# Performance work log

Hardware: AMD Instinct MI355X
Metric: run time of the kernel (lower is better)

The kernel has to match this reference:

```python
import jax, jax.numpy as jnp
import numpy as np

N = 50000      # nodes
E = 1_000_000  # edges (avg degree 20)
D = 64         # hidden dim
L = 3          # num dynamics layers
LN_EPS = 1e-5


def layernorm(h, g, b):
    mu = jnp.mean(h, axis=-1, keepdims=True)
    var = jnp.mean(jnp.square(h - mu), axis=-1, keepdims=True)
    return (h - mu) * jax.lax.rsqrt(var + LN_EPS) * g + b


def transformer_conv(h, src, dst, Wq, bq, Wk, bk, Wv, bv, Ws, bs):
    # PyG TransformerConv, heads=1, concat=False, beta=False, root_weight=True
    n = h.shape[0]
    d = Wq.shape[1]
    q = h @ Wq + bq            # [N, D] queries (dst side)
    k = h @ Wk + bk            # [N, D] keys   (src side)
    v = h @ Wv + bv            # [N, D] values (src side)
    logits = jnp.sum(q[dst] * k[src], axis=-1) / jnp.sqrt(jnp.asarray(d, h.dtype))  # [E]
    # segment softmax over incoming edges of each dst node
    m = jax.ops.segment_max(logits, dst, num_segments=n)      # [N]
    e = jnp.exp(logits - m[dst])                               # [E]
    s = jax.ops.segment_sum(e, dst, num_segments=n)            # [N]
    a = e / s[dst]                                             # [E]
    agg = jax.ops.segment_sum(a[:, None] * v[src], dst, num_segments=n)  # [N, D]
    return agg + h @ Ws + bs   # root/skip connection


def setup_inputs() -> dict:
    key = jax.random.key(0)
    ks = jax.random.split(key, 24)
    w = lambda k, shape: (jax.random.normal(k, shape, jnp.float32) * 0.05)
    inp = {
        "x": jax.random.normal(ks[0], (N, D), jnp.float32),
        "edge_index": jax.random.randint(ks[1], (2, E), 0, N, jnp.int32),
        # input_proj conv params
        "Wq0": w(ks[2], (D, D)), "bq0": w(ks[3], (D,)),
        "Wk0": w(ks[4], (D, D)), "bk0": w(ks[5], (D,)),
        "Wv0": w(ks[6], (D, D)), "bv0": w(ks[7], (D,)),
        "Ws0": w(ks[8], (D, D)), "bs0": w(ks[9], (D,)),
        "ln0_g": jnp.ones((D,), jnp.float32), "ln0_b": jnp.zeros((D,), jnp.float32),
        # stacked dynamics conv params [L, ...]
        "Wq": w(ks[10], (L, D, D)), "bq": w(ks[11], (L, D)),
        "Wk": w(ks[12], (L, D, D)), "bk": w(ks[13], (L, D)),
        "Wv": w(ks[14], (L, D, D)), "bv": w(ks[15], (L, D)),
        "Ws": w(ks[16], (L, D, D)), "bs": w(ks[17], (L, D)),
        "ln_g": jnp.ones((L, D), jnp.float32), "ln_b": jnp.zeros((L, D), jnp.float32),
    }
    return inp


def reference(x, edge_index, Wq0, bq0, Wk0, bk0, Wv0, bv0, Ws0, bs0, ln0_g, ln0_b,
              Wq, bq, Wk, bk, Wv, bv, Ws, bs, ln_g, ln_b):
    src, dst = edge_index[0], edge_index[1]
    h = transformer_conv(x, src, dst, Wq0, bq0, Wk0, bk0, Wv0, bv0, Ws0, bs0)
    h = jax.nn.relu(layernorm(h, ln0_g, ln0_b))
    # dropout is identity in eval mode
    for i in range(L):
        hi = transformer_conv(h, src, dst, Wq[i], bq[i], Wk[i], bk[i],
                              Wv[i], bv[i], Ws[i], bs[i])
        h = jax.nn.relu(layernorm(hi + h, ln_g[i], ln_b[i]))
    return h
```

## Files before the change

### kernel.cpp

```cpp
#include <hip/hip_runtime.h>
#include <math.h>

#define NN 50000
#define NE 1000000
#define CAP 64
#define LN_EPS 1e-5f
#define ROW_TILES 3125
#define BE_T 250112

typedef __attribute__((ext_vector_type(8))) short short8;
typedef __attribute__((ext_vector_type(8))) unsigned short ushort8;
typedef __attribute__((ext_vector_type(4))) float f32x4;

__device__ __forceinline__ unsigned short f2bf(float f) {
  union { float f; unsigned u; } v; v.f = f;
  unsigned r = v.u + 0x7FFF + ((v.u >> 16) & 1);
  return (unsigned short)(r >> 16);
}
__device__ __forceinline__ float bf2f(unsigned short b) {
  union { unsigned u; float f; } v; v.u = ((unsigned)b) << 16;
  return v.f;
}

__global__ __launch_bounds__(256) void build_ell(const int* __restrict__ ei,
                                                 int* __restrict__ cursor,
                                                 unsigned short* __restrict__ ell) {
  int t = blockIdx.x * 256 + threadIdx.x;
  int e[4]; bool v[4]; int s[4], d[4], p[4];
#pragma unroll
  for (int i = 0; i < 4; ++i) { e[i] = t + i * BE_T; v[i] = e[i] < NE; }
#pragma unroll
  for (int i = 0; i < 4; ++i) {
    if (v[i]) { s[i] = ei[e[i]]; d[i] = ei[NE + e[i]]; }
  }
#pragma unroll
  for (int i = 0; i < 4; ++i) {
    if (v[i]) p[i] = atomicAdd(&cursor[d[i]], 1);
  }
#pragma unroll
  for (int i = 0; i < 4; ++i) {
    if (v[i] && p[i] < CAP) ell[(size_t)d[i] * CAP + p[i]] = (unsigned short)s[i];
  }
}

__global__ __launch_bounds__(256) void wprep(
    const float* __restrict__ Wq0, const float* __restrict__ bq0,
    const float* __restrict__ Wk0, const float* __restrict__ bk0,
    const float* __restrict__ Wv0, const float* __restrict__ bv0,
    const float* __restrict__ Ws0, const float* __restrict__ bs0,
    const float* __restrict__ WqL, const float* __restrict__ bqL,
    const float* __restrict__ WkL, const float* __restrict__ bkL,
    const float* __restrict__ WvL, const float* __restrict__ bvL,
    const float* __restrict__ WsL, const float* __restrict__ bsL,
    unsigned short* __restrict__ Wt, float* __restrict__ Bc) {
  int tid = blockIdx.x * 256 + threadIdx.x;
  if (tid >= 4 * 256 * 64) return;
  int lyr = tid >> 14;
  int rem = tid & 16383;
  int c = rem >> 6;
  int k = rem & 63;
  int m = c >> 6;
  int n = c & 63;
  const float *W, *B;
  if (lyr == 0) {
    const float* Wm[4] = {Wq0, Wk0, Wv0, Ws0};
    const float* Bm[4] = {bq0, bk0, bv0, bs0};
    W = Wm[m]; B = Bm[m];
  } else {
    const float* Wm[4] = {WqL, WkL, WvL, WsL};
    const float* Bm[4] = {bqL, bkL, bvL, bsL};
    W = Wm[m] + (size_t)(lyr - 1) * 4096;
    B = Bm[m] + (size_t)(lyr - 1) * 64;
  }
  Wt[(size_t)lyr * 16384 + (size_t)c * 64 + k] = f2bf(W[(size_t)k * 64 + n]);
  if (k == 0) Bc[lyr * 256 + c] = B[n];
}

__global__ __launch_bounds__(256) void gemm_qkvs(
    const float* __restrict__ h, const unsigned short* __restrict__ Wt,
    const float* __restrict__ Bc, float* __restrict__ Qf,
    unsigned int* __restrict__ KVb, float* __restrict__ Sf) {
  __shared__ unsigned short lw[256 * 72];
  int tid = threadIdx.x;
#pragma unroll
  for (int it = 0; it < 8; ++it) {
    int id = it * 256 + tid;
    int row = id >> 3, cc = id & 7;
    float4 src = *reinterpret_cast<const float4*>(Wt + (size_t)row * 64 + cc * 8);
    *reinterpret_cast<float4*>(lw + (size_t)row * 72 + cc * 8) = src;
  }
  __syncthreads();

  int wave = tid >> 6, lane = tid & 63;
  int tile = blockIdx.x * 4 + wave;
  if (tile >= ROW_TILES) return;
  int lo = lane & 15, hi = lane >> 4;
  int row = tile * 16 + lo;
  const float* hrow = h + (size_t)row * 64;

  auto packA = [&](const float* p) {
    float4 x = *reinterpret_cast<const float4*>(p);
    float4 y = *reinterpret_cast<const float4*>(p + 4);
    short8 r;
    r[0] = (short)f2bf(x.x); r[1] = (short)f2bf(x.y);
    r[2] = (short)f2bf(x.z); r[3] = (short)f2bf(x.w);
    r[4] = (short)f2bf(y.x); r[5] = (short)f2bf(y.y);
    r[6] = (short)f2bf(y.z); r[7] = (short)f2bf(y.w);
    return r;
  };
  short8 a0 = packA(hrow + hi * 8);
  short8 a1 = packA(hrow + 32 + hi * 8);

  int rb = tile * 16 + hi * 4;

  auto mm = [&](int brow, float bias) {
    f32x4 acc = {bias, bias, bias, bias};
    const unsigned short* wr = lw + (size_t)brow * 72 + hi * 8;
    short8 b0 = *reinterpret_cast<const short8*>(wr);
    short8 b1 = *reinterpret_cast<const short8*>(wr + 32);
    acc = __builtin_amdgcn_mfma_f32_16x16x32_bf16(a0, b0, acc, 0, 0, 0);
    acc = __builtin_amdgcn_mfma_f32_16x16x32_bf16(a1, b1, acc, 0, 0, 0);
    return acc;
  };

#pragma unroll
  for (int ct = 0; ct < 4; ++ct) {
    int col = ct * 16 + lo;
    f32x4 acc = mm(col, Bc[col]);
#pragma unroll
    for (int r = 0; r < 4; ++r) Qf[(size_t)(rb + r) * 64 + col] = acc[r];
  }
#pragma unroll
  for (int cg = 0; cg < 4; ++cg) {
    int col = cg * 16 + lo;
    f32x4 aK = mm(64 + col, Bc[64 + col]);
    f32x4 aV = mm(128 + col, Bc[128 + col]);
#pragma unroll
    for (int r = 0; r < 4; ++r) {
      unsigned int pk = (unsigned int)f2bf(aK[r]) | ((unsigned int)f2bf(aV[r]) << 16);
      KVb[(size_t)(rb + r) * 64 + col] = pk;
    }
  }
#pragma unroll
  for (int ct = 0; ct < 4; ++ct) {
    int col = ct * 16 + lo;
    f32x4 acc = mm(192 + col, Bc[192 + col]);
#pragma unroll
    for (int r = 0; r < 4; ++r) Sf[(size_t)(rb + r) * 64 + col] = acc[r];
  }
}

__global__ __launch_bounds__(256) void edge_fused(
    const float* __restrict__ Qf, const unsigned short* __restrict__ KVb,
    const float* __restrict__ Sf,
    const unsigned short* __restrict__ ell, const int* __restrict__ cursor,
    const float* __restrict__ ln_g, const float* __restrict__ ln_b,
    const float* __restrict__ h_res, float* __restrict__ h_out, int use_res) {
  int node = blockIdx.x * 4 + (threadIdx.x >> 6);
  if (node >= NN) return;
  int lane = threadIdx.x & 63;
  int g = lane >> 4, t = lane & 15;

  int deg = cursor[node];
  if (deg > CAP) deg = CAP;
  const unsigned short* lst = ell + (size_t)node * CAP;

  float4 q4 = *reinterpret_cast<const float4*>(Qf + (size_t)node * 64 + t * 4);

  float4 acc = {0.f, 0.f, 0.f, 0.f};
  float ssum = 0.f;
  int passes = (deg + 3) >> 2;
  for (int p = 0; p < passes; ++p) {
    int slot = p * 4 + g;
    bool valid = slot < deg;
    int src = valid ? (int)lst[slot] : 0;
    ushort8 kv = *reinterpret_cast<const ushort8*>(KVb + (size_t)src * 128 + t * 8);
    float dp = q4.x * bf2f(kv[0]) + q4.y * bf2f(kv[2]) +
               q4.z * bf2f(kv[4]) + q4.w * bf2f(kv[6]);
    dp += __shfl_xor(dp, 1, 64);
    dp += __shfl_xor(dp, 2, 64);
    dp += __shfl_xor(dp, 4, 64);
    dp += __shfl_xor(dp, 8, 64);
    float w = valid ? __expf(dp * 0.125f) : 0.f;
    ssum += w;
    acc.x = fmaf(w, bf2f(kv[1]), acc.x);
    acc.y = fmaf(w, bf2f(kv[3]), acc.y);
    acc.z = fmaf(w, bf2f(kv[5]), acc.z);
    acc.w = fmaf(w, bf2f(kv[7]), acc.w);
  }
#pragma unroll
  for (int off = 16; off <= 32; off <<= 1) {
    acc.x += __shfl_xor(acc.x, off, 64);
    acc.y += __shfl_xor(acc.y, off, 64);
    acc.z += __shfl_xor(acc.z, off, 64);
    acc.w += __shfl_xor(acc.w, off, 64);
    ssum  += __shfl_xor(ssum, off, 64);
  }
  float inv = (ssum > 0.f) ? (1.f / ssum) : 0.f;

  float4 s4 = *reinterpret_cast<const float4*>(Sf + (size_t)node * 64 + t * 4);
  float4 o;
  o.x = acc.x * inv + s4.x;
  o.y = acc.y * inv + s4.y;
  o.z = acc.z * inv + s4.z;
  o.w = acc.w * inv + s4.w;
  if (use_res) {
    float4 r4 = *reinterpret_cast<const float4*>(h_res + (size_t)node * 64 + t * 4);
    o.x += r4.x; o.y += r4.y; o.z += r4.z; o.w += r4.w;
  }

  float sum = o.x + o.y + o.z + o.w;
  sum += __shfl_xor(sum, 1, 64);
  sum += __shfl_xor(sum, 2, 64);
  sum += __shfl_xor(sum, 4, 64);
  sum += __shfl_xor(sum, 8, 64);
  float mu = sum * (1.f / 64.f);
  float dx = o.x - mu, dy = o.y - mu, dz = o.z - mu, dw = o.w - mu;
  float vs = dx * dx + dy * dy + dz * dz + dw * dw;
  vs += __shfl_xor(vs, 1, 64);
  vs += __shfl_xor(vs, 2, 64);
  vs += __shfl_xor(vs, 4, 64);
  vs += __shfl_xor(vs, 8, 64);
  float rstd = rsqrtf(vs * (1.f / 64.f) + LN_EPS);
  float4 gg = *reinterpret_cast<const float4*>(ln_g + t * 4);
  float4 bb = *reinterpret_cast<const float4*>(ln_b + t * 4);
  float4 y;
  y.x = fmaxf(dx * rstd * gg.x + bb.x, 0.f);
  y.y = fmaxf(dy * rstd * gg.y + bb.y, 0.f);
  y.z = fmaxf(dz * rstd * gg.z + bb.z, 0.f);
  y.w = fmaxf(dw * rstd * gg.w + bb.w, 0.f);
  *reinterpret_cast<float4*>(h_out + (size_t)node * 64 + t * 4) = y;
}

extern "C" void kernel_launch(void* const* d_in, const int* in_sizes, int n_in,
                              void* d_out, int out_size, void* d_ws, size_t ws_size,
                              hipStream_t stream) {
  const float* x    = (const float*)d_in[0];
  const int*   ei   = (const int*)d_in[1];
  const float* Wq0  = (const float*)d_in[2];
  const float* bq0  = (const float*)d_in[3];
  const float* Wk0  = (const float*)d_in[4];
  const float* bk0  = (const float*)d_in[5];
  const float* Wv0  = (const float*)d_in[6];
  const float* bv0  = (const float*)d_in[7];
  const float* Ws0  = (const float*)d_in[8];
  const float* bs0  = (const float*)d_in[9];
  const float* ln0g = (const float*)d_in[10];
  const float* ln0b = (const float*)d_in[11];
  const float* WqL  = (const float*)d_in[12];
  const float* bqL  = (const float*)d_in[13];
  const float* WkL  = (const float*)d_in[14];
  const float* bkL  = (const float*)d_in[15];
  const float* WvL  = (const float*)d_in[16];
  const float* bvL  = (const float*)d_in[17];
  const float* WsL  = (const float*)d_in[18];
  const float* bsL  = (const float*)d_in[19];
  const float* lnG  = (const float*)d_in[20];
  const float* lnB  = (const float*)d_in[21];

  float* h = (float*)d_out;

  char* ws = (char*)d_ws;
  size_t off = 0;
  float* Qf = (float*)(ws + off);                    off += (size_t)NN * 64 * 4;
  float* Sf = (float*)(ws + off);                    off += (size_t)NN * 64 * 4;
  unsigned int* KVb = (unsigned int*)(ws + off);     off += (size_t)NN * 128 * 2;
  unsigned short* ell = (unsigned short*)(ws + off); off += (size_t)NN * CAP * 2;
  int* cursor = (int*)(ws + off);                    off += (size_t)NN * 4;
  unsigned short* Wt = (unsigned short*)(ws + off);  off += (size_t)4 * 256 * 64 * 2;
  float* Bc = (float*)(ws + off);                    off += (size_t)4 * 256 * 4;

  hipMemsetAsync(cursor, 0, NN * sizeof(int), stream);
  build_ell<<<BE_T / 256, 256, 0, stream>>>(ei, cursor, ell);
  wprep<<<256, 256, 0, stream>>>(Wq0, bq0, Wk0, bk0, Wv0, bv0, Ws0, bs0,
                                 WqL, bqL, WkL, bkL, WvL, bvL, WsL, bsL, Wt, Bc);

  for (int layer = 0; layer < 4; ++layer) {
    const float* hin = (layer == 0) ? x : h;
    const float* lg = (layer == 0) ? ln0g : lnG + (size_t)(layer - 1) * 64;
    const float* lb = (layer == 0) ? ln0b : lnB + (size_t)(layer - 1) * 64;
    gemm_qkvs<<<(ROW_TILES + 3) / 4, 256, 0, stream>>>(
        hin, Wt + (size_t)layer * 16384, Bc + (size_t)layer * 256, Qf, KVb, Sf);
    edge_fused<<<(NN + 3) / 4, 256, 0, stream>>>(
        Qf, (const unsigned short*)KVb, Sf, ell, cursor, lg, lb, h, h,
        layer > 0 ? 1 : 0);
  }
}
```

Before: 423.7 us.

## Fuse ELL build into first GEMM, store Q as bf16, prefetch KV

Merges the edge-list build into the layer-0 QKVS GEMM launch as extra blocks, so graph construction can overlap with the projection and one launch is dropped. Queries are now stored in bf16 instead of fp32, halving Q traffic. The edge aggregation loop software-pipelines neighbor K/V loads two passes ahead to hide gather latency. The costs are lower precision in the attention logits and higher register pressure in the edge kernel.

```diff
diff --git a/kernel.cpp b/kernel.cpp
--- a/kernel.cpp
+++ b/kernel.cpp
@@ -6,7 +6,9 @@
 #define CAP 64
 #define LN_EPS 1e-5f
 #define ROW_TILES 3125
+#define GEMM_BLOCKS 782
 #define BE_T 250112
+#define ELL_BLOCKS 977
 
 typedef __attribute__((ext_vector_type(8))) short short8;
 typedef __attribute__((ext_vector_type(8))) unsigned short ushort8;
@@ -20,27 +22,6 @@
 __device__ __forceinline__ float bf2f(unsigned short b) {
   union { unsigned u; float f; } v; v.u = ((unsigned)b) << 16;
   return v.f;
-}
-
-__global__ __launch_bounds__(256) void build_ell(const int* __restrict__ ei,
-                                                 int* __restrict__ cursor,
-                                                 unsigned short* __restrict__ ell) {
-  int t = blockIdx.x * 256 + threadIdx.x;
-  int e[4]; bool v[4]; int s[4], d[4], p[4];
-#pragma unroll
-  for (int i = 0; i < 4; ++i) { e[i] = t + i * BE_T; v[i] = e[i] < NE; }
-#pragma unroll
-  for (int i = 0; i < 4; ++i) {
-    if (v[i]) { s[i] = ei[e[i]]; d[i] = ei[NE + e[i]]; }
-  }
-#pragma unroll
-  for (int i = 0; i < 4; ++i) {
-    if (v[i]) p[i] = atomicAdd(&cursor[d[i]], 1);
-  }
-#pragma unroll
-  for (int i = 0; i < 4; ++i) {
-    if (v[i] && p[i] < CAP) ell[(size_t)d[i] * CAP + p[i]] = (unsigned short)s[i];
-  }
 }
 
 __global__ __launch_bounds__(256) void wprep(
@@ -78,10 +59,33 @@
 
 __global__ __launch_bounds__(256) void gemm_qkvs(
     const float* __restrict__ h, const unsigned short* __restrict__ Wt,
-    const float* __restrict__ Bc, float* __restrict__ Qf,
-    unsigned int* __restrict__ KVb, float* __restrict__ Sf) {
+    const float* __restrict__ Bc, unsigned short* __restrict__ Qb,
+    unsigned int* __restrict__ KVb, float* __restrict__ Sf,
+    const int* __restrict__ ei, int* __restrict__ cursor,
+    unsigned short* __restrict__ ell, int nGemm) {
   __shared__ unsigned short lw[256 * 72];
   int tid = threadIdx.x;
+
+  if ((int)blockIdx.x >= nGemm) {
+    int t = (blockIdx.x - nGemm) * 256 + tid;
+    int e[4]; bool v[4]; int s[4], d[4], p[4];
+#pragma unroll
+    for (int i = 0; i < 4; ++i) { e[i] = t + i * BE_T; v[i] = e[i] < NE; }
+#pragma unroll
+    for (int i = 0; i < 4; ++i) {
+      if (v[i]) { s[i] = ei[e[i]]; d[i] = ei[NE + e[i]]; }
+    }
+#pragma unroll
+    for (int i = 0; i < 4; ++i) {
+      if (v[i]) p[i] = atomicAdd(&cursor[d[i]], 1);
+    }
+#pragma unroll
+    for (int i = 0; i < 4; ++i) {
+      if (v[i] && p[i] < CAP) ell[(size_t)d[i] * CAP + p[i]] = (unsigned short)s[i];
+    }
+    return;
+  }
+
 #pragma unroll
   for (int it = 0; it < 8; ++it) {
     int id = it * 256 + tid;
@@ -128,7 +132,7 @@
     int col = ct * 16 + lo;
     f32x4 acc = mm(col, Bc[col]);
 #pragma unroll
-    for (int r = 0; r < 4; ++r) Qf[(size_t)(rb + r) * 64 + col] = acc[r];
+    for (int r = 0; r < 4; ++r) Qb[(size_t)(rb + r) * 64 + col] = f2bf(acc[r]);
   }
 #pragma unroll
   for (int cg = 0; cg < 4; ++cg) {
@@ -151,7 +155,7 @@
 }
 
 __global__ __launch_bounds__(256) void edge_fused(
-    const float* __restrict__ Qf, const unsigned short* __restrict__ KVb,
+    const unsigned short* __restrict__ Qb, const unsigned short* __restrict__ KVb,
     const float* __restrict__ Sf,
     const unsigned short* __restrict__ ell, const int* __restrict__ cursor,
     const float* __restrict__ ln_g, const float* __restrict__ ln_b,
@@ -165,28 +169,37 @@
   if (deg > CAP) deg = CAP;
   const unsigned short* lst = ell + (size_t)node * CAP;
 
-  float4 q4 = *reinterpret_cast<const float4*>(Qf + (size_t)node * 64 + t * 4);
+  ushort4 qv = *reinterpret_cast<const ushort4*>(Qb + (size_t)node * 64 + t * 4);
+  float q0 = bf2f(qv.x), q1 = bf2f(qv.y), q2 = bf2f(qv.z), q3 = bf2f(qv.w);
+
+  int passes = (deg + 3) >> 2;
+
+  auto ldkv = [&](int p) {
+    int slot = p * 4 + g;
+    int src = (slot < deg) ? (int)lst[slot] : 0;
+    return *reinterpret_cast<const ushort8*>(KVb + (size_t)src * 128 + t * 8);
+  };
 
   float4 acc = {0.f, 0.f, 0.f, 0.f};
   float ssum = 0.f;
-  int passes = (deg + 3) >> 2;
+  ushort8 b0 = ldkv(0);
+  ushort8 b1 = ldkv(1);
   for (int p = 0; p < passes; ++p) {
-    int slot = p * 4 + g;
-    bool valid = slot < deg;
-    int src = valid ? (int)lst[slot] : 0;
-    ushort8 kv = *reinterpret_cast<const ushort8*>(KVb + (size_t)src * 128 + t * 8);
-    float dp = q4.x * bf2f(kv[0]) + q4.y * bf2f(kv[2]) +
-               q4.z * bf2f(kv[4]) + q4.w * bf2f(kv[6]);
+    ushort8 b2 = ldkv(p + 2);
+    bool valid = (p * 4 + g) < deg;
+    float dp = q0 * bf2f(b0[0]) + q1 * bf2f(b0[2]) +
+               q2 * bf2f(b0[4]) + q3 * bf2f(b0[6]);
     dp += __shfl_xor(dp, 1, 64);
     dp += __shfl_xor(dp, 2, 64);
     dp += __shfl_xor(dp, 4, 64);
     dp += __shfl_xor(dp, 8, 64);
     float w = valid ? __expf(dp * 0.125f) : 0.f;
     ssum += w;
-    acc.x = fmaf(w, bf2f(kv[1]), acc.x);
-    acc.y = fmaf(w, bf2f(kv[3]), acc.y);
-    acc.z = fmaf(w, bf2f(kv[5]), acc.z);
-    acc.w = fmaf(w, bf2f(kv[7]), acc.w);
+    acc.x = fmaf(w, bf2f(b0[1]), acc.x);
+    acc.y = fmaf(w, bf2f(b0[3]), acc.y);
+    acc.z = fmaf(w, bf2f(b0[5]), acc.z);
+    acc.w = fmaf(w, bf2f(b0[7]), acc.w);
+    b0 = b1; b1 = b2;
   }
 #pragma unroll
   for (int off = 16; off <= 32; off <<= 1) {
@@ -262,7 +275,7 @@
 
   char* ws = (char*)d_ws;
   size_t off = 0;
-  float* Qf = (float*)(ws + off);                    off += (size_t)NN * 64 * 4;
+  unsigned short* Qb = (unsigned short*)(ws + off);  off += (size_t)NN * 64 * 2;
   float* Sf = (float*)(ws + off);                    off += (size_t)NN * 64 * 4;
   unsigned int* KVb = (unsigned int*)(ws + off);     off += (size_t)NN * 128 * 2;
   unsigned short* ell = (unsigned short*)(ws + off); off += (size_t)NN * CAP * 2;
@@ -271,7 +284,6 @@
   float* Bc = (float*)(ws + off);                    off += (size_t)4 * 256 * 4;
 
   hipMemsetAsync(cursor, 0, NN * sizeof(int), stream);
-  build_ell<<<BE_T / 256, 256, 0, stream>>>(ei, cursor, ell);
   wprep<<<256, 256, 0, stream>>>(Wq0, bq0, Wk0, bk0, Wv0, bv0, Ws0, bs0,
                                  WqL, bqL, WkL, bkL, WvL, bvL, WsL, bsL, Wt, Bc);
 
@@ -279,10 +291,12 @@
     const float* hin = (layer == 0) ? x : h;
     const float* lg = (layer == 0) ? ln0g : lnG + (size_t)(layer - 1) * 64;
     const float* lb = (layer == 0) ? ln0b : lnB + (size_t)(layer - 1) * 64;
-    gemm_qkvs<<<(ROW_TILES + 3) / 4, 256, 0, stream>>>(
-        hin, Wt + (size_t)layer * 16384, Bc + (size_t)layer * 256, Qf, KVb, Sf);
+    int extra = (layer == 0) ? ELL_BLOCKS : 0;
+    gemm_qkvs<<<GEMM_BLOCKS + extra, 256, 0, stream>>>(
+        hin, Wt + (size_t)layer * 16384, Bc + (size_t)layer * 256,
+        Qb, KVb, Sf, ei, cursor, ell, GEMM_BLOCKS);
     edge_fused<<<(NN + 3) / 4, 256, 0, stream>>>(
-        Qf, (const unsigned short*)KVb, Sf, ell, cursor, lg, lb, h, h,
+        Qb, (const unsigned short*)KVb, Sf, ell, cursor, lg, lb, h, h,
         layer > 0 ? 1 : 0);
   }
 }
```

Result: faster. 392.5 us (-7.4%).
